# Optimization experiments

Hardware: AMD Instinct MI355X
Metric: run time of the kernel (lower is better)

Reference implementation:

```python
import jax, jax.numpy as jnp
import numpy as np

V = 50257      # num_class
H = 512        # hid_size
EMB = 256      # embedding_size
E = 128        # emb_cond_size
COND_RANGE = (10, 20, 30)
NCSEQ = 100    # num_cond_seq_class
T, B = 64, 32
TC = 32        # cond_seq length


def _gru_scan(x, h0, Wih, Whh, bih, bhh):
    """PyTorch-convention GRU. x: [T,B,in], h0: [B,Hd]. Gate order: r,z,n."""
    Hd = h0.shape[-1]
    xw = jnp.einsum('tbi,gi->tbg', x, Wih) + bih  # [T,B,3H]

    def step(h, xw_t):
        hw = h @ Whh.T + bhh
        r = jax.nn.sigmoid(xw_t[:, :Hd] + hw[:, :Hd])
        z = jax.nn.sigmoid(xw_t[:, Hd:2 * Hd] + hw[:, Hd:2 * Hd])
        n = jnp.tanh(xw_t[:, 2 * Hd:] + r * hw[:, 2 * Hd:])
        hn = (1.0 - z) * n + z * h
        return hn, hn

    hT, outs = jax.lax.scan(step, h0, xw)
    return outs, hT


def setup_inputs() -> dict:
    key = jax.random.key(0)
    ks = jax.random.split(key, 24)
    s = 0.02
    inp = {
        'input_data': jax.random.randint(ks[0], (T, B), 0, V),
        'condition': jnp.stack([jax.random.randint(ks[1 + i], (B,), 0, COND_RANGE[i]) for i in range(3)], 0),
        'cond_seq': jax.random.randint(ks[4], (TC, B), 0, NCSEQ),
        'emb_cond_0': jax.random.normal(ks[5], (COND_RANGE[0], E)) * s,
        'emb_cond_1': jax.random.normal(ks[6], (COND_RANGE[1], E)) * s,
        'emb_cond_2': jax.random.normal(ks[7], (COND_RANGE[2], E)) * s,
        'cond_seq_emb': jax.random.normal(ks[8], (NCSEQ, E)) * s,
        'embedding': jax.random.normal(ks[9], (V, EMB)) * s,
        'attn_W': jax.random.normal(ks[10], (H, E + H)) * s,
        'attn_b': jnp.zeros((H,), jnp.float32),
        'v_W': jax.random.normal(ks[11], (1, H)) * s,
        'gru_Wih': jax.random.normal(ks[12], (3 * H, EMB)) * s,
        'gru_Whh': jax.random.normal(ks[13], (3 * H, H)) * s,
        'gru_bih': jnp.zeros((3 * H,), jnp.float32),
        'gru_bhh': jnp.zeros((3 * H,), jnp.float32),
        'cgru_Wih': jax.random.normal(ks[14], (3 * E, E)) * s,
        'cgru_Whh': jax.random.normal(ks[15], (3 * E, E)) * s,
        'cgru_bih': jnp.zeros((3 * E,), jnp.float32),
        'cgru_bhh': jnp.zeros((3 * E,), jnp.float32),
        'dense_W': jax.random.normal(ks[16], (V, E + EMB + H)) * s,
        'dense_b': jnp.zeros((V,), jnp.float32),
    }
    return inp


def reference(input_data, condition, cond_seq,
              emb_cond_0, emb_cond_1, emb_cond_2, cond_seq_emb, embedding,
              attn_W, attn_b, v_W,
              gru_Wih, gru_Whh, gru_bih, gru_bhh,
              cgru_Wih, cgru_Whh, cgru_bih, cgru_bhh,
              dense_W, dense_b):
    Tl, Bl = input_data.shape
    # conditional embeddings: [num_cond, B, E]
    tables = (emb_cond_0, emb_cond_1, emb_cond_2)
    cond_emb = jnp.stack([tables[i][condition[i]] for i in range(3)], axis=0)
    # conditional sequence GRU encoder: [TC, B, E]
    cseq_in = cond_seq_emb[cond_seq]
    cseq_out, _ = _gru_scan(cseq_in, jnp.zeros((Bl, E), cseq_in.dtype),
                            cgru_Wih, cgru_Whh, cgru_bih, cgru_bhh)
    enc = jnp.concatenate([cond_emb, cseq_out], axis=0)  # [S, B, E]
    enc_b = jnp.transpose(enc, (1, 0, 2))                # [B, S, E]

    # Bahdanau attention: split attn weight into encoder/decoder parts
    W_e = attn_W[:, :E]   # [H, E]
    W_h = attn_W[:, E:]   # [H, H]
    enc_proj = jnp.einsum('bse,he->bsh', enc_b, W_e)     # precompute once

    x_emb = embedding[input_data]                        # [T, B, EMB]
    xw = jnp.einsum('tbi,gi->tbg', x_emb, gru_Wih) + gru_bih  # [T, B, 3H]

    def step(h, inputs):
        xe_t, xw_t = inputs
        # attention against previous hidden h
        score = jnp.tanh(enc_proj + (h @ W_h.T + attn_b)[:, None, :]) @ v_W[0]  # [B,S]
        w = jax.nn.softmax(score, axis=1)
        c = jnp.einsum('bs,bse->be', w, enc_b)           # [B, E]
        # GRU cell
        hw = h @ gru_Whh.T + gru_bhh
        r = jax.nn.sigmoid(xw_t[:, :H] + hw[:, :H])
        z = jax.nn.sigmoid(xw_t[:, H:2 * H] + hw[:, H:2 * H])
        n = jnp.tanh(xw_t[:, 2 * H:] + r * hw[:, 2 * H:])
        hn = (1.0 - z) * n + z * h
        # output head uses context, input embedding and PREVIOUS hidden h
        logits = jnp.concatenate([c, xe_t, h], axis=-1) @ dense_W.T + dense_b
        pred = jax.nn.log_softmax(logits, axis=-1)
        return hn, (pred, w)

    h0 = jnp.zeros((Bl, H), x_emb.dtype)
    hT, (total_pred, weights) = jax.lax.scan(step, h0, (x_emb, xw))
    return total_pred, hT[None, :, :], weights


if __name__ == '__main__':
    out = reference(**setup_inputs())
    print([o.shape for o in out])
```

## Files before the change

### kernel.cpp

```cpp
#include <hip/hip_runtime.h>
#include <hip/hip_bf16.h>
#include <hip/hip_cooperative_groups.h>
#include <math.h>

namespace cg = cooperative_groups;

#define Tt 64
#define Bb 32
#define Hh 512
#define EMBe 256
#define Ee 128
#define Ss 35
#define Vv 50257
#define Kk 896
#define TCc 32
#define VPAD 50304

typedef __bf16 bf16_t;
typedef __bf16 bf16x4 __attribute__((ext_vector_type(4)));
typedef __bf16 bf16x8 __attribute__((ext_vector_type(8)));
typedef float f32x4 __attribute__((ext_vector_type(4)));

__device__ __forceinline__ float sigf(float x){ return 1.f/(1.f + expf(-x)); }

__device__ __forceinline__ void gll16(const void* g, void* l){
  __builtin_amdgcn_global_load_lds(
      (const __attribute__((address_space(1))) unsigned int*)g,
      (__attribute__((address_space(3))) unsigned int*)l, 16, 0, 0);
}

#define DOT4(acc, W_, H_) acc += (W_).x*(H_).x + (W_).y*(H_).y + (W_).z*(H_).z + (W_).w*(H_).w

__global__ void k_cond_emb(const int* __restrict__ cond, const float* __restrict__ t0,
                           const float* __restrict__ t1, const float* __restrict__ t2,
                           float* __restrict__ enc){
  int g = blockIdx.x*blockDim.x + threadIdx.x;
  if (g >= 3*Bb*Ee) return;
  int i = g/(Bb*Ee); int b = (g/Ee)%Bb; int e = g%Ee;
  const float* tbl = (i==0)? t0 : (i==1)? t1 : t2;
  int ci = cond[i*Bb + b];
  enc[(size_t)i*Bb*Ee + b*Ee + e] = tbl[(size_t)ci*Ee + e];
}

__global__ void k_cxw(const int* __restrict__ cond_seq, const float* __restrict__ cemb,
                      const float* __restrict__ Wih, const float* __restrict__ bih,
                      float* __restrict__ cxw){
  __shared__ float es[Ee];
  int row = blockIdx.x; int tid = threadIdx.x;
  int idx = cond_seq[row];
  es[tid] = cemb[(size_t)idx*Ee + tid];
  __syncthreads();
  const float4* hp = (const float4*)es;
  for (int q = 0; q < 3; ++q){
    int g = q*Ee + tid;
    const float4* wr = (const float4*)(Wih + (size_t)g*Ee);
    float acc = bih[g];
    #pragma unroll 8
    for (int k = 0; k < Ee/4; ++k){ float4 w4 = wr[k]; float4 h4 = hp[k]; DOT4(acc, w4, h4); }
    cxw[(size_t)row*(3*Ee) + g] = acc;
  }
}

__global__ void k_xemb(const int* __restrict__ input_data, const float* __restrict__ emb,
                       bf16_t* __restrict__ xe){
  int row = blockIdx.x, tid = threadIdx.x;
  int idx = input_data[row];
  xe[(size_t)row*EMBe + tid] = (bf16_t)emb[(size_t)idx*EMBe + tid];
}

__global__ void k_ctrans(const float* __restrict__ W, float* __restrict__ WT){
  int idx = blockIdx.x*256 + threadIdx.x;
  if (idx >= 3*Ee*Ee) return;
  int g = idx/Ee, k = idx%Ee;
  WT[(size_t)k*(3*Ee) + g] = W[idx];
}

__global__ void k_cseq_scan(const float* __restrict__ cxw, const float* __restrict__ WT,
                            const float* __restrict__ bhh, float* __restrict__ enc){
  __shared__ float hs[Ee];
  int b = blockIdx.x; int j = threadIdx.x;
  hs[j] = 0.f; __syncthreads();
  float b0 = bhh[j], b1 = bhh[Ee+j], b2 = bhh[2*Ee+j];
  for (int t = 0; t < TCc; ++t){
    const float* xp = cxw + ((size_t)t*Bb + b)*(3*Ee);
    float a0=b0, a1=b1, a2=b2;
    #pragma unroll 4
    for (int k = 0; k < Ee; ++k){
      float hk = hs[k];
      const float* wr = WT + (size_t)k*(3*Ee);
      a0 += hk * wr[j];
      a1 += hk * wr[Ee + j];
      a2 += hk * wr[2*Ee + j];
    }
    float r = sigf(xp[j] + a0);
    float z = sigf(xp[Ee + j] + a1);
    float n = tanhf(xp[2*Ee + j] + r*a2);
    float hcur = hs[j];
    float hn = (1.f - z)*n + z*hcur;
    __syncthreads();
    hs[j] = hn;
    enc[(size_t)(3+t)*Bb*Ee + b*Ee + j] = hn;
    __syncthreads();
  }
}

__global__ void k_encproj(const float* __restrict__ enc, const float* __restrict__ attn_W,
                          float* __restrict__ enc_proj){
  __shared__ float es[Ee];
  int blk = blockIdx.x; int tid = threadIdx.x;
  int b = blk/Ss, s = blk%Ss;
  if (tid < Ee) es[tid] = enc[(size_t)s*Bb*Ee + b*Ee + tid];
  __syncthreads();
  const float4* hp = (const float4*)es;
  for (int q = 0; q < 2; ++q){
    int hh = q*256 + tid;
    const float4* wr = (const float4*)(attn_W + (size_t)hh*(Ee+Hh));
    float acc = 0.f;
    #pragma unroll 8
    for (int k = 0; k < Ee/4; ++k){ float4 w4 = wr[k]; float4 h4 = hp[k]; DOT4(acc, w4, h4); }
    enc_proj[(size_t)blk*Hh + hh] = acc;
  }
}

__global__ void k_binit(int* bar){
  int i = threadIdx.x;
  if (i < 256)
    __hip_atomic_store(&bar[i], 0, __ATOMIC_RELAXED, __HIP_MEMORY_SCOPE_AGENT);
}

#define SCAN_BLOCKS 16
#define SCAN_THREADS 384
#define WSL_STRIDE 520
#define HST_STRIDE 520
#define GW_STRIDE 104
#define HSLOT (Bb*Hh)
#define SCAN_LDS (96*WSL_STRIDE*2 + Bb*HST_STRIDE*2 + Bb*GW_STRIDE*4)

__device__ __forceinline__ void poll16(const int* flags, int gen){
  const int* p = flags + ((threadIdx.x & 15))*16;
  for (;;){
    int v = __hip_atomic_load(p, __ATOMIC_RELAXED, __HIP_MEMORY_SCOPE_AGENT);
    if (__all(v >= gen)) break;
    __builtin_amdgcn_s_sleep(1);
  }
}

__global__ __launch_bounds__(SCAN_THREADS) void k_scan_coop(
    const float* __restrict__ xw, const float* __restrict__ Whh,
    const float* __restrict__ bhh, float* __restrict__ h_all,
    bf16_t* __restrict__ hsteps, int* __restrict__ bar){
  extern __shared__ char smem[];
  bf16_t* Wsl = (bf16_t*)smem;
  bf16_t* hst = (bf16_t*)(smem + 96*WSL_STRIDE*2);
  float*  gw  = (float*) (smem + 96*WSL_STRIDE*2 + Bb*HST_STRIDE*2);
  const int tid = threadIdx.x;
  const int blk = blockIdx.x;
  const int c0 = blk*32;
  int* wflag = bar;

  for (int lr = 0; lr < 96; ++lr){
    int g = lr >> 5, i = lr & 31;
    const float* src = Whh + ((size_t)g*Hh + c0 + i)*Hh;
    for (int c = tid; c < Hh; c += SCAN_THREADS)
      Wsl[lr*WSL_STRIDE + c] = (bf16_t)src[c];
  }
  for (int idx = tid; idx < Bb*16; idx += SCAN_THREADS){
    int b = idx >> 4, u = idx & 15;
    __hip_atomic_store((unsigned*)hsteps + ((b*Hh + c0) >> 1) + u, 0u,
                       __ATOMIC_RELAXED, __HIP_MEMORY_SCOPE_AGENT);
    float* hp = &h_all[(size_t)b*Hh + c0 + u*2];
    hp[0] = 0.f; hp[1] = 0.f;
  }

  const int npair = (tid < 128) ? 2 : 1;
  int pb[2], pc[2];
  float bh0[2][2], bh1[2][2], bh2[2][2], hreg[2][2];
  for (int p = 0; p < npair; ++p){
    int pid = tid + p*SCAN_THREADS;
    pb[p] = pid >> 4; pc[p] = (pid & 15)*2;
    for (int c = 0; c < 2; ++c){
      int j = c0 + pc[p] + c;
      bh0[p][c] = bhh[j]; bh1[p][c] = bhh[Hh + j]; bh2[p][c] = bhh[2*Hh + j];
      hreg[p][c] = 0.f;
    }
  }

  __syncthreads();
  if (tid == 0)
    __hip_atomic_store(&wflag[blk*16], 1, __ATOMIC_RELAXED, __HIP_MEMORY_SCOPE_AGENT);

  const int wid = tid >> 6, lane = tid & 63;
  const int l15 = lane & 15, l4 = lane >> 4;

  for (int t = 0; t < Tt; ++t){
    poll16(wflag, t + 1);
    {
      const unsigned long long* hinU = (const unsigned long long*)(hsteps + (size_t)t*HSLOT);
      for (int idx = tid; idx < Bb*Hh/4; idx += SCAN_THREADS){
        unsigned long long v = __hip_atomic_load(hinU + idx, __ATOMIC_RELAXED, __HIP_MEMORY_SCOPE_AGENT);
        int b = idx >> 7, c4 = idx & 127;
        *((unsigned long long*)(hst + (size_t)b*HST_STRIDE) + c4) = v;
      }
    }
    __syncthreads();

    f32x4 acc0 = {0.f,0.f,0.f,0.f}, acc1 = {0.f,0.f,0.f,0.f};
    #pragma unroll
    for (int ks = 0; ks < 16; ++ks){
      bf16x8 bfr = *(const bf16x8*)(Wsl + (wid*16 + l15)*WSL_STRIDE + ks*32 + l4*8);
      bf16x8 a0  = *(const bf16x8*)(hst + l15*HST_STRIDE        + ks*32 + l4*8);
      bf16x8 a1  = *(const bf16x8*)(hst + (16 + l15)*HST_STRIDE + ks*32 + l4*8);
      acc0 = __builtin_amdgcn_mfma_f32_16x16x32_bf16(a0, bfr, acc0, 0, 0, 0);
      acc1 = __builtin_amdgcn_mfma_f32_16x16x32_bf16(a1, bfr, acc1, 0, 0, 0);
    }
    #pragma unroll
    for (int i = 0; i < 4; ++i){
      gw[(l4*4 + i)*GW_STRIDE + wid*16 + l15]        = acc0[i];
      gw[(16 + l4*4 + i)*GW_STRIDE + wid*16 + l15]   = acc1[i];
    }
    __syncthreads();

    unsigned* houtU = (unsigned*)(hsteps + (size_t)(t+1)*HSLOT);
    for (int p = 0; p < npair; ++p){
      int b = pb[p], cl = pc[p];
      const float* xp = xw + ((size_t)t*Bb + b)*(3*Hh);
      float hn2[2];
      #pragma unroll
      for (int c = 0; c < 2; ++c){
        int j = c0 + cl + c;
        float gr = gw[b*GW_STRIDE + cl + c]      + bh0[p][c];
        float gz = gw[b*GW_STRIDE + 32 + cl + c] + bh1[p][c];
        float gn = gw[b*GW_STRIDE + 64 + cl + c] + bh2[p][c];
        float r = sigf(xp[j] + gr);
        float z = sigf(xp[Hh + j] + gz);
        float n = tanhf(xp[2*Hh + j] + r*gn);
        float hn = (1.f - z)*n + z*hreg[p][c];
        hreg[p][c] = hn; hn2[c] = hn;
      }
      unsigned u0 = (unsigned)__builtin_bit_cast(unsigned short, (bf16_t)hn2[0]);
      unsigned u1 = (unsigned)__builtin_bit_cast(unsigned short, (bf16_t)hn2[1]);
      __hip_atomic_store(houtU + ((b*Hh + c0 + cl) >> 1), u0 | (u1 << 16),
                         __ATOMIC_RELAXED, __HIP_MEMORY_SCOPE_AGENT);
    }
    __syncthreads();
    if (tid == 0 && t + 1 < Tt)
      __hip_atomic_store(&wflag[blk*16], t + 2, __ATOMIC_RELAXED, __HIP_MEMORY_SCOPE_AGENT);
    for (int p = 0; p < npair; ++p){
      int b = pb[p], cl = pc[p];
      float* hp = &h_all[((size_t)(t+1)*Bb + b)*Hh + c0 + cl];
      hp[0] = hreg[p][0]; hp[1] = hreg[p][1];
    }
  }
}

#define SG_LDS (256*64*2)
#define SWZ(rowv, uv) (((size_t)(rowv))*64 + ((((uv) ^ ((rowv)&7)))<<3))

template<int KTOT, int LDB>
__global__ __launch_bounds__(256) void k_sgemm(const bf16_t* __restrict__ A,
                                               const float* __restrict__ B,
                                               const float* __restrict__ bias,
                                               float* __restrict__ C, int N){
  extern __shared__ char smem[];
  bf16_t* As = (bf16_t*)smem;
  bf16_t* Ws = As + 128*64;
  const int tid = threadIdx.x, bid = blockIdx.x;
  const int mt = bid & 15, nt = bid >> 4;
  const int m0 = mt*128, n0 = nt*128;
  const int srow = tid >> 1, sub = (tid & 1)*4;
  const int NKK2 = KTOT/64;

  int4 aR[4]; float4 wF[8];
#define SLOADA(KK) { \
    const int4* p = (const int4*)(A + (size_t)(m0 + srow)*KTOT + (KK)*64 + sub*8); \
    aR[0]=p[0]; aR[1]=p[1]; aR[2]=p[2]; aR[3]=p[3]; }
#define SLOADW(KK) { \
    const float4* p = (const float4*)(B + (size_t)(n0 + srow)*LDB + (KK)*64 + sub*8); \
    _Pragma("unroll") for (int r = 0; r < 8; ++r) wF[r] = p[r]; }
#define SSTORES() { \
    _Pragma("unroll") \
    for (int j = 0; j < 4; ++j) \
      *(int4*)(As + SWZ(srow, sub + j)) = aR[j]; \
    _Pragma("unroll") for (int j = 0; j < 4; ++j){ \
      bf16x8 p8; \
      p8[0]=(bf16_t)wF[2*j].x; p8[1]=(bf16_t)wF[2*j].y; p8[2]=(bf16_t)wF[2*j].z; p8[3]=(bf16_t)wF[2*j].w; \
      p8[4]=(bf16_t)wF[2*j+1].x; p8[5]=(bf16_t)wF[2*j+1].y; p8[6]=(bf16_t)wF[2*j+1].z; p8[7]=(bf16_t)wF[2*j+1].w; \
      *(bf16x8*)(Ws + SWZ(srow, sub + j)) = p8; \
    } }

  const int wave = tid >> 6, lane = tid & 63;
  const int l15 = lane & 15, l4 = lane >> 4;
  const int mh = (wave >> 1)*64, nh = (wave & 1)*64;

  f32x4 acc[4][4];
  #pragma unroll
  for (int i = 0; i < 4; ++i)
    #pragma unroll
    for (int j = 0; j < 4; ++j) acc[i][j] = (f32x4){0.f,0.f,0.f,0.f};

  SLOADA(0); SLOADW(0);
  SSTORES();
  __syncthreads();
  for (int kk = 0; kk < NKK2; ++kk){
    if (kk + 1 < NKK2){ SLOADA(kk + 1); SLOADW(kk + 1); }
    #pragma unroll
    for (int k32 = 0; k32 < 2; ++k32){
      const int u = k32*4 + l4;
      bf16x8 aF[4], bF[4];
      #pragma unroll
      for (int mf = 0; mf < 4; ++mf)
        aF[mf] = *(const bf16x8*)(As + SWZ(mh + mf*16 + l15, u));
      #pragma unroll
      for (int nf = 0; nf < 4; ++nf)
        bF[nf] = *(const bf16x8*)(Ws + SWZ(nh + nf*16 + l15, u));
      #pragma unroll
      for (int mf = 0; mf < 4; ++mf)
        #pragma unroll
        for (int nf = 0; nf < 4; ++nf)
          acc[mf][nf] = __builtin_amdgcn_mfma_f32_16x16x32_bf16(aF[mf], bF[nf], acc[mf][nf], 0, 0, 0);
    }
    __syncthreads();
    if (kk + 1 < NKK2){
      SSTORES();
      __syncthreads();
    }
  }
  #pragma unroll
  for (int mf = 0; mf < 4; ++mf){
    #pragma unroll
    for (int nf = 0; nf < 4; ++nf){
      int v = n0 + nh + nf*16 + l15;
      float bv = bias[v];
      int m = m0 + mh + mf*16 + l4*4;
      #pragma unroll
      for (int i = 0; i < 4; ++i)
        C[(size_t)(m + i)*N + v] = acc[mf][nf][i] + bv;
    }
  }
#undef SLOADA
#undef SLOADW
#undef SSTORES
}

__global__ void k_score(const float* __restrict__ hw_attn, const float* __restrict__ enc_proj,
                        const float* __restrict__ enc, const float* __restrict__ vW,
                        float* __restrict__ w_out, float* __restrict__ c_all){
  __shared__ float hws[Hh];
  __shared__ float sc[Ss];
  __shared__ float wsm[Ss];
  int row = blockIdx.x, lane = threadIdx.x;
  int b = row & (Bb-1);
  for (int k = lane; k < Hh; k += 64) hws[k] = hw_attn[(size_t)row*Hh + k];
  __syncthreads();
  for (int s = 0; s < Ss; ++s){
    const float* ep = enc_proj + ((size_t)b*Ss + s)*Hh;
    float acc = 0.f;
    for (int k = lane; k < Hh; k += 64) acc += tanhf(ep[k] + hws[k]) * vW[k];
    #pragma unroll
    for (int off = 32; off > 0; off >>= 1) acc += __shfl_xor(acc, off);
    if (lane == 0) sc[s] = acc;
  }
  __syncthreads();
  float val = (lane < Ss) ? sc[lane] : -3.0e38f;
  float mx = val;
  #pragma unroll
  for (int off = 32; off > 0; off >>= 1) mx = fmaxf(mx, __shfl_xor(mx, off));
  float e = (lane < Ss) ? expf(val - mx) : 0.f;
  float sm = e;
  #pragma unroll
  for (int off = 32; off > 0; off >>= 1) sm += __shfl_xor(sm, off);
  float w = e / sm;
  if (lane < Ss){ w_out[(size_t)row*Ss + lane] = w; wsm[lane] = w; }
  __syncthreads();
  for (int q = 0; q < 2; ++q){
    int ee = q*64 + lane;
    float acc = 0.f;
    #pragma unroll
    for (int s = 0; s < Ss; ++s) acc += wsm[s]*enc[(size_t)s*Bb*Ee + b*Ee + ee];
    c_all[(size_t)row*Ee + ee] = acc;
  }
}

__global__ void k_abuild(const int* __restrict__ input_data, const float* __restrict__ c_all,
                         const float* __restrict__ embedding, const float* __restrict__ h_all,
                         bf16_t* __restrict__ A){
  int row = blockIdx.x, tid = threadIdx.x;
  int xidx = input_data[row];
  bf16_t* Ar = A + (size_t)row*Kk;
  int rs = row & 7;
  for (int col = tid; col < Kk; col += 256){
    float v;
    if (col < Ee) v = c_all[(size_t)row*Ee + col];
    else if (col < Ee + EMBe) v = embedding[(size_t)xidx*EMBe + (col - Ee)];
    else v = h_all[(size_t)row*Hh + (col - Ee - EMBe)];
    int kk = col >> 6, u = (col & 63) >> 3, e = col & 7;
    Ar[(kk << 6) + ((u ^ rs) << 3) + e] = (bf16_t)v;
  }
}

__global__ void k_wconv(const float* __restrict__ Wd, bf16_t* __restrict__ Wb){
  size_t i = ((size_t)blockIdx.x*256 + threadIdx.x)*8;
  if (i >= (size_t)VPAD*Kk) return;
  size_t row = i / Kk;
  int col = (int)(i % Kk);
  bf16x8 o;
  if (row < Vv){
    float4 f0 = *(const float4*)(Wd + i);
    float4 f1 = *(const float4*)(Wd + i + 4);
    o[0]=(bf16_t)f0.x; o[1]=(bf16_t)f0.y; o[2]=(bf16_t)f0.z; o[3]=(bf16_t)f0.w;
    o[4]=(bf16_t)f1.x; o[5]=(bf16_t)f1.y; o[6]=(bf16_t)f1.z; o[7]=(bf16_t)f1.w;
  } else {
    #pragma unroll
    for (int k = 0; k < 8; ++k) o[k] = (bf16_t)0.f;
  }
  int kk = col >> 6, u = (col & 63) >> 3;
  int rs = (int)(row & 7);
  *(bf16x8*)(Wb + row*Kk + (kk << 6) + ((u ^ rs) << 3)) = o;
}

#define BM 128
#define BN 128
#define BK 64
#define NKK (Kk/BK)
#define GEMM_LDS ((BM + BN)*BK*2)

template<int WBF>
__global__ __launch_bounds__(256) void k_gemm7(const bf16_t* __restrict__ A,
                                               const void* __restrict__ Wsrc,
                                               const float* __restrict__ bias,
                                               float* __restrict__ out){
  extern __shared__ char smem[];
  bf16_t* As = (bf16_t*)smem;
  bf16_t* Ws = As + BM*BK;
  const int tid = threadIdx.x;
  const int bid = blockIdx.x;
  const int mt = bid & 15, nt = bid >> 4;
  const int m0 = mt*BM, n0 = nt*BN;
  const int wave = tid >> 6, lane = tid & 63;
  const int l15 = lane & 15, l4 = lane >> 4;
  const int mh = (wave >> 1)*64, nh = (wave & 1)*64;

  f32x4 acc[4][4];
  #pragma unroll
  for (int i = 0; i < 4; ++i)
    #pragma unroll
    for (int j = 0; j < 4; ++j) acc[i][j] = (f32x4){0.f,0.f,0.f,0.f};

  if (WBF){
    const char* Ag = (const char*)A;
    const char* Wg = (const char*)Wsrc;
    char* Asb = (char*)As; char* Wsb = (char*)Ws;
    const int grow = tid >> 3;
    const size_t gcol = (size_t)(tid & 7)*16;
    #pragma unroll
    for (int j = 0; j < 4; ++j){
      gll16(Ag + (size_t)(m0 + j*32 + grow)*(Kk*2) + gcol, Asb + j*4096 + tid*16);
      gll16(Wg + (size_t)(n0 + j*32 + grow)*(Kk*2) + gcol, Wsb + j*4096 + tid*16);
    }
    __syncthreads();
    for (int kk = 0; kk < NKK; ++kk){
      #pragma unroll
      for (int k32 = 0; k32 < 2; ++k32){
        const int u = k32*4 + l4;
        bf16x8 aF[4], bF[4];
        #pragma unroll
        for (int mf = 0; mf < 4; ++mf)
          aF[mf] = *(const bf16x8*)(As + SWZ(mh + mf*16 + l15, u));
        #pragma unroll
        for (int nf = 0; nf < 4; ++nf)
          bF[nf] = *(const bf16x8*)(Ws + SWZ(nh + nf*16 + l15, u));
        #pragma unroll
        for (int mf = 0; mf < 4; ++mf)
          #pragma unroll
          for (int nf = 0; nf < 4; ++nf)
            acc[mf][nf] = __builtin_amdgcn_mfma_f32_16x16x32_bf16(aF[mf], bF[nf], acc[mf][nf], 0, 0, 0);
      }
      __syncthreads();
      if (kk + 1 < NKK){
        size_t ko = (size_t)(kk + 1)*128;
        #pragma unroll
        for (int j = 0; j < 4; ++j){
          gll16(Ag + (size_t)(m0 + j*32 + grow)*(Kk*2) + ko + gcol, Asb + j*4096 + tid*16);
          gll16(Wg + (size_t)(n0 + j*32 + grow)*(Kk*2) + ko + gcol, Wsb + j*4096 + tid*16);
        }
        __syncthreads();
      }
    }
  } else {
    const int srow = tid >> 1, sub = (tid & 1)*4;
    int4 aR[4]; float4 wF[8];
    const float* Wf = (const float*)Wsrc;
#define LOADA(KK) { \
    const int4* p = (const int4*)(A + (size_t)(m0 + srow)*Kk + (KK)*BK + sub*8); \
    aR[0]=p[0]; aR[1]=p[1]; aR[2]=p[2]; aR[3]=p[3]; }
#define LOADW(KK) { \
    int vrow = n0 + srow; \
    if (vrow < Vv){ \
      const float4* p = (const float4*)(Wf + (size_t)vrow*Kk + (KK)*BK + sub*8); \
      _Pragma("unroll") for (int r = 0; r < 8; ++r) wF[r] = p[r]; \
    } else { \
      _Pragma("unroll") for (int r = 0; r < 8; ++r) wF[r] = make_float4(0.f,0.f,0.f,0.f); \
    } }
#define STORES() { \
    _Pragma("unroll") \
    for (int j = 0; j < 4; ++j) \
      *(int4*)(As + (size_t)srow*64 + (size_t)(sub + j)*8) = aR[j]; \
    _Pragma("unroll") for (int j = 0; j < 4; ++j){ \
      bf16x8 p8; \
      p8[0]=(bf16_t)wF[2*j].x; p8[1]=(bf16_t)wF[2*j].y; p8[2]=(bf16_t)wF[2*j].z; p8[3]=(bf16_t)wF[2*j].w; \
      p8[4]=(bf16_t)wF[2*j+1].x; p8[5]=(bf16_t)wF[2*j+1].y; p8[6]=(bf16_t)wF[2*j+1].z; p8[7]=(bf16_t)wF[2*j+1].w; \
      *(bf16x8*)(Ws + SWZ(srow, sub + j)) = p8; \
    } }
    LOADA(0); LOADW(0);
    STORES();
    __syncthreads();
    for (int kk = 0; kk < NKK; ++kk){
      if (kk + 1 < NKK){ LOADA(kk + 1); LOADW(kk + 1); }
      #pragma unroll
      for (int k32 = 0; k32 < 2; ++k32){
        const int u = k32*4 + l4;
        bf16x8 aF[4], bF[4];
        #pragma unroll
        for (int mf = 0; mf < 4; ++mf)
          aF[mf] = *(const bf16x8*)(As + SWZ(mh + mf*16 + l15, u));
        #pragma unroll
        for (int nf = 0; nf < 4; ++nf)
          bF[nf] = *(const bf16x8*)(Ws + SWZ(nh + nf*16 + l15, u));
        #pragma unroll
        for (int mf = 0; mf < 4; ++mf)
          #pragma unroll
          for (int nf = 0; nf < 4; ++nf)
            acc[mf][nf] = __builtin_amdgcn_mfma_f32_16x16x32_bf16(aF[mf], bF[nf], acc[mf][nf], 0, 0, 0);
      }
      __syncthreads();
      if (kk + 1 < NKK){
        STORES();
        __syncthreads();
      }
    }
#undef LOADA
#undef LOADW
#undef STORES
  }
  #pragma unroll
  for (int mf = 0; mf < 4; ++mf){
    #pragma unroll
    for (int nf = 0; nf < 4; ++nf){
      int v = n0 + nh + nf*16 + l15;
      if (v < Vv){
        float bv = bias[v];
        int m = m0 + mh + mf*16 + l4*4;
        #pragma unroll
        for (int i = 0; i < 4; ++i){
          out[(size_t)(m + i)*Vv + v] = acc[mf][nf][i] + bv;
        }
      }
    }
  }
}

__global__ void k_lse(const float* __restrict__ pred, float* __restrict__ lse){
  __shared__ float ms[256], ssum[256];
  int row = blockIdx.x, tid = threadIdx.x;
  const float* p = pred + (size_t)row*Vv;
  int pre = (int)(((16 - (((size_t)p) & 15)) & 15) >> 2);
  float m = -3.0e38f, s = 0.f;
  if (tid < pre){ float x = p[tid]; m = x; s = 1.f; }
  int n4 = (Vv - pre) >> 2;
  const float4* p4 = (const float4*)(p + pre);
  for (int v = tid; v < n4; v += 256){
    float4 x4 = p4[v];
    #pragma unroll
    for (int q = 0; q < 4; ++q){
      float x = (q==0)? x4.x : (q==1)? x4.y : (q==2)? x4.z : x4.w;
      if (x > m){ s = s*expf(m - x) + 1.f; m = x; }
      else s += expf(x - m);
    }
  }
  int tl = pre + n4*4 + tid;
  if (tl < Vv){ float x = p[tl]; if (x > m){ s = s*expf(m - x) + 1.f; m = x; } else s += expf(x - m); }
  ms[tid] = m; ssum[tid] = s;
  __syncthreads();
  for (int off = 128; off > 0; off >>= 1){
    if (tid < off){
      float m2 = ms[tid+off], s2 = ssum[tid+off];
      float m1 = ms[tid],     s1 = ssum[tid];
      if (m2 > m1){ s1 = s1*expf(m1 - m2) + s2; m1 = m2; }
      else s1 += s2*expf(m2 - m1);
      ms[tid] = m1; ssum[tid] = s1;
    }
    __syncthreads();
  }
  if (tid == 0) lse[row] = ms[0] + logf(ssum[0]);
}

__global__ void k_sub(float* __restrict__ pred, const float* __restrict__ lse){
  int row = blockIdx.x, tid = threadIdx.x;
  float l = lse[row];
  float* p = pred + (size_t)row*Vv;
  int pre = (int)(((16 - (((size_t)p) & 15)) & 15) >> 2);
  if (tid < pre) p[tid] -= l;
  int n4 = (Vv - pre) >> 2;
  float4* p4 = (float4*)(p + pre);
  for (int v = tid; v < n4; v += 256){
    float4 x = p4[v];
    x.x -= l; x.y -= l; x.z -= l; x.w -= l;
    p4[v] = x;
  }
  int tl = pre + n4*4 + tid;
  if (tl < Vv) p[tl] -= l;
}

__global__ void k_hT(const float* __restrict__ h_all, float* __restrict__ hT){
  int g = blockIdx.x*256 + threadIdx.x;
  if (g < Bb*Hh) hT[g] = h_all[(size_t)Tt*Bb*Hh + g];
}

extern "C" void kernel_launch(void* const* d_in, const int* in_sizes, int n_in,
                              void* d_out, int out_size, void* d_ws, size_t ws_size,
                              hipStream_t stream){
  const int*   input_data = (const int*)d_in[0];
  const int*   condition  = (const int*)d_in[1];
  const int*   cond_seq   = (const int*)d_in[2];
  const float* emb_c0     = (const float*)d_in[3];
  const float* emb_c1     = (const float*)d_in[4];
  const float* emb_c2     = (const float*)d_in[5];
  const float* cseq_emb   = (const float*)d_in[6];
  const float* embedding  = (const float*)d_in[7];
  const float* attn_W     = (const float*)d_in[8];
  const float* attn_b     = (const float*)d_in[9];
  const float* v_W        = (const float*)d_in[10];
  const float* gru_Wih    = (const float*)d_in[11];
  const float* gru_Whh    = (const float*)d_in[12];
  const float* gru_bih    = (const float*)d_in[13];
  const float* gru_bhh    = (const float*)d_in[14];
  const float* cgru_Wih   = (const float*)d_in[15];
  const float* cgru_Whh   = (const float*)d_in[16];
  const float* cgru_bih   = (const float*)d_in[17];
  const float* cgru_bhh   = (const float*)d_in[18];
  const float* dense_W    = (const float*)d_in[19];
  const float* dense_b    = (const float*)d_in[20];

  float* out    = (float*)d_out;
  float* pred   = out;
  float* hT_out = out + (size_t)Tt*Bb*Vv;
  float* w_out  = hT_out + (size_t)Bb*Hh;

  float* ws       = (float*)d_ws;
  float* h_all    = ws;
  float* xw       = h_all + (size_t)(Tt+1)*Bb*Hh;
  float* cxw      = xw + (size_t)Tt*Bb*3*Hh;
  float* enc      = cxw + (size_t)TCc*Bb*3*Ee;
  float* enc_proj = enc + (size_t)Ss*Bb*Ee;
  float* hw_attn  = enc_proj + (size_t)Bb*Ss*Hh;
  float* c_all    = hw_attn + (size_t)Tt*Bb*Hh;
  float* lse      = c_all + (size_t)Tt*Bb*Ee;
  bf16_t* Abf     = (bf16_t*)(lse + Tt*Bb);
  bf16_t* hsteps  = Abf + (size_t)Tt*Bb*Kk;
  float* WTc      = (float*)(hsteps + (size_t)(Tt+1)*HSLOT);
  int*   bar      = (int*)(WTc + 128*3*Ee);
  bf16_t* xemb    = (bf16_t*)(bar + 256);
  bf16_t* Wb      = xemb + (size_t)Tt*Bb*EMBe;
  size_t need_b   = (size_t)((char*)(Wb + (size_t)VPAD*Kk) - (char*)d_ws);
  bool use_wbf    = (ws_size >= need_b);

  k_cond_emb<<<48, 256, 0, stream>>>(condition, emb_c0, emb_c1, emb_c2, enc);
  k_cxw<<<TCc*Bb, 128, 0, stream>>>(cond_seq, cseq_emb, cgru_Wih, cgru_bih, cxw);
  k_xemb<<<Tt*Bb, 256, 0, stream>>>(input_data, embedding, xemb);
  k_sgemm<EMBe, EMBe><<<16*12, 256, SG_LDS, stream>>>(xemb, gru_Wih, gru_bih, xw, 3*Hh);
  k_ctrans<<<(3*Ee*Ee + 255)/256, 256, 0, stream>>>(cgru_Whh, WTc);
  k_cseq_scan<<<Bb, Ee, 0, stream>>>(cxw, WTc, cgru_bhh, enc);
  k_encproj<<<Bb*Ss, 256, 0, stream>>>(enc, attn_W, enc_proj);
  k_binit<<<1, 256, 0, stream>>>(bar);
  if (use_wbf)
    k_wconv<<<(int)(((size_t)VPAD*Kk/8 + 255)/256), 256, 0, stream>>>(dense_W, Wb);

  (void)hipFuncSetAttribute((const void*)k_scan_coop, hipFuncAttributeMaxDynamicSharedMemorySize, SCAN_LDS);
  {
    void* xw_p = (void*)xw; void* whh_p = (void*)gru_Whh; void* bhh_p = (void*)gru_bhh;
    void* ha_p = (void*)h_all; void* hs_p = (void*)hsteps; void* bar_p = (void*)bar;
    void* args[] = {&xw_p, &whh_p, &bhh_p, &ha_p, &hs_p, &bar_p};
    (void)hipLaunchCooperativeKernel((const void*)k_scan_coop, dim3(SCAN_BLOCKS), dim3(SCAN_THREADS),
                                     args, SCAN_LDS, stream);
  }

  k_sgemm<Hh, (Ee+Hh)><<<16*4, 256, SG_LDS, stream>>>(hsteps, attn_W + Ee, attn_b, hw_attn, Hh);
  k_score<<<Tt*Bb, 64, 0, stream>>>(hw_attn, enc_proj, enc, v_W, w_out, c_all);
  k_abuild<<<Tt*Bb, 256, 0, stream>>>(input_data, c_all, embedding, h_all, Abf);

  (void)hipFuncSetAttribute((const void*)k_gemm7<1>, hipFuncAttributeMaxDynamicSharedMemorySize, GEMM_LDS);
  (void)hipFuncSetAttribute((const void*)k_gemm7<0>, hipFuncAttributeMaxDynamicSharedMemorySize, GEMM_LDS);
  if (use_wbf){
    k_gemm7<1><<<16*((Vv + BN - 1)/BN), 256, GEMM_LDS, stream>>>(Abf, (const void*)Wb, dense_b, pred);
  } else {
    k_gemm7<0><<<16*((Vv + BN - 1)/BN), 256, GEMM_LDS, stream>>>(Abf, (const void*)dense_W, dense_b, pred);
  }

  k_lse<<<Tt*Bb, 256, 0, stream>>>(pred, lse);
  k_sub<<<Tt*Bb, 256, 0, stream>>>(pred, lse);
  k_hT<<<64, 256, 0, stream>>>(h_all, hT_out);
}
```

Measured before the change: 1.777 ms.

## Replace scan flag barrier with NaN-poison polling and overlap dense weight conversion

Drops the per-step flag barrier in the cooperative GRU scan. The hidden-state buffer is now pre-filled with a NaN sentinel, and each block spin-waits on the data itself until the sentinel is overwritten. The dense weight fp32-to-bf16 conversion moves into extra blocks of the same cooperative launch, so it runs concurrently with the 16 latency-bound scan blocks instead of as a separate kernel. The cost is a poison pass over 65 hidden slots, and the scheme relies on a real hidden value never bit-matching the sentinel pattern.

```diff
diff --git a/kernel.cpp b/kernel.cpp
--- a/kernel.cpp
+++ b/kernel.cpp
@@ -20,6 +20,8 @@
 typedef __bf16 bf16x4 __attribute__((ext_vector_type(4)));
 typedef __bf16 bf16x8 __attribute__((ext_vector_type(8)));
 typedef float f32x4 __attribute__((ext_vector_type(4)));
+
+#define POIS32 0x7FC07FC0u
 
 __device__ __forceinline__ float sigf(float x){ return 1.f/(1.f + expf(-x)); }
 
@@ -122,41 +124,64 @@
   }
 }
 
-__global__ void k_binit(int* bar){
-  int i = threadIdx.x;
-  if (i < 256)
-    __hip_atomic_store(&bar[i], 0, __ATOMIC_RELAXED, __HIP_MEMORY_SCOPE_AGENT);
-}
-
-#define SCAN_BLOCKS 16
+#define HSLOT (Bb*Hh)
+
+__global__ void k_poison(bf16_t* __restrict__ hsteps){
+  size_t i = (size_t)blockIdx.x*256 + threadIdx.x;
+  size_t total = (size_t)(Tt+1)*HSLOT/2;
+  if (i >= total) return;
+  unsigned v = (i < HSLOT/2) ? 0u : POIS32;
+  __hip_atomic_store((unsigned*)hsteps + i, v, __ATOMIC_RELAXED, __HIP_MEMORY_SCOPE_AGENT);
+}
+
+#define SCAN_BLOCKS_L 128
+#define SCAN_WORK 16
 #define SCAN_THREADS 384
 #define WSL_STRIDE 520
 #define HST_STRIDE 520
 #define GW_STRIDE 104
-#define HSLOT (Bb*Hh)
 #define SCAN_LDS (96*WSL_STRIDE*2 + Bb*HST_STRIDE*2 + Bb*GW_STRIDE*4)
-
-__device__ __forceinline__ void poll16(const int* flags, int gen){
-  const int* p = flags + ((threadIdx.x & 15))*16;
-  for (;;){
-    int v = __hip_atomic_load(p, __ATOMIC_RELAXED, __HIP_MEMORY_SCOPE_AGENT);
-    if (__all(v >= gen)) break;
-    __builtin_amdgcn_s_sleep(1);
-  }
-}
+#define NCH 11
 
 __global__ __launch_bounds__(SCAN_THREADS) void k_scan_coop(
     const float* __restrict__ xw, const float* __restrict__ Whh,
     const float* __restrict__ bhh, float* __restrict__ h_all,
-    bf16_t* __restrict__ hsteps, int* __restrict__ bar){
+    bf16_t* __restrict__ hsteps, const float* __restrict__ Wd,
+    bf16_t* __restrict__ Wb, int wbf){
   extern __shared__ char smem[];
+  const int tid = threadIdx.x;
+  const int blk = blockIdx.x;
+
+  if (blk >= SCAN_WORK){
+    if (wbf){
+      size_t total = (size_t)VPAD*Kk/8;
+      size_t stride = (size_t)(SCAN_BLOCKS_L - SCAN_WORK)*SCAN_THREADS;
+      for (size_t c = (size_t)(blk - SCAN_WORK)*SCAN_THREADS + tid; c < total; c += stride){
+        size_t i = c*8;
+        size_t row = i / Kk;
+        int col = (int)(i % Kk);
+        bf16x8 o;
+        if (row < Vv){
+          float4 f0 = *(const float4*)(Wd + i);
+          float4 f1 = *(const float4*)(Wd + i + 4);
+          o[0]=(bf16_t)f0.x; o[1]=(bf16_t)f0.y; o[2]=(bf16_t)f0.z; o[3]=(bf16_t)f0.w;
+          o[4]=(bf16_t)f1.x; o[5]=(bf16_t)f1.y; o[6]=(bf16_t)f1.z; o[7]=(bf16_t)f1.w;
+        } else {
+          #pragma unroll
+          for (int k = 0; k < 8; ++k) o[k] = (bf16_t)0.f;
+        }
+        int kk = col >> 6, u = (col & 63) >> 3;
+        int rs = (int)(row & 7);
+        *(bf16x8*)(Wb + row*Kk + (kk << 6) + ((u ^ rs) << 3)) = o;
+      }
+    }
+    return;
+  }
+
   bf16_t* Wsl = (bf16_t*)smem;
   bf16_t* hst = (bf16_t*)(smem + 96*WSL_STRIDE*2);
   float*  gw  = (float*) (smem + 96*WSL_STRIDE*2 + Bb*HST_STRIDE*2);
-  const int tid = threadIdx.x;
-  const int blk = blockIdx.x;
   const int c0 = blk*32;
-  int* wflag = bar;
 
   for (int lr = 0; lr < 96; ++lr){
     int g = lr >> 5, i = lr & 31;
@@ -166,8 +191,6 @@
   }
   for (int idx = tid; idx < Bb*16; idx += SCAN_THREADS){
     int b = idx >> 4, u = idx & 15;
-    __hip_atomic_store((unsigned*)hsteps + ((b*Hh + c0) >> 1) + u, 0u,
-                       __ATOMIC_RELAXED, __HIP_MEMORY_SCOPE_AGENT);
     float* hp = &h_all[(size_t)b*Hh + c0 + u*2];
     hp[0] = 0.f; hp[1] = 0.f;
   }
@@ -184,22 +207,41 @@
       hreg[p][c] = 0.f;
     }
   }
-
   __syncthreads();
-  if (tid == 0)
-    __hip_atomic_store(&wflag[blk*16], 1, __ATOMIC_RELAXED, __HIP_MEMORY_SCOPE_AGENT);
 
   const int wid = tid >> 6, lane = tid & 63;
   const int l15 = lane & 15, l4 = lane >> 4;
 
   for (int t = 0; t < Tt; ++t){
-    poll16(wflag, t + 1);
     {
       const unsigned long long* hinU = (const unsigned long long*)(hsteps + (size_t)t*HSLOT);
-      for (int idx = tid; idx < Bb*Hh/4; idx += SCAN_THREADS){
-        unsigned long long v = __hip_atomic_load(hinU + idx, __ATOMIC_RELAXED, __HIP_MEMORY_SCOPE_AGENT);
-        int b = idx >> 7, c4 = idx & 127;
-        *((unsigned long long*)(hst + (size_t)b*HST_STRIDE) + c4) = v;
+      unsigned long long v[NCH];
+      int nmine = 0;
+      #pragma unroll
+      for (int k = 0; k < NCH; ++k){
+        int idx = tid + k*SCAN_THREADS;
+        if (idx < Bb*Hh/4){
+          v[k] = __hip_atomic_load(hinU + idx, __ATOMIC_RELAXED, __HIP_MEMORY_SCOPE_AGENT);
+          nmine = k + 1;
+        }
+      }
+      #pragma unroll
+      for (int k = 0; k < NCH; ++k){
+        if (k < nmine){
+          int idx = tid + k*SCAN_THREADS;
+          while ((unsigned)v[k] == POIS32 || (unsigned)(v[k] >> 32) == POIS32){
+            __builtin_amdgcn_s_sleep(1);
+            v[k] = __hip_atomic_load(hinU + idx, __ATOMIC_RELAXED, __HIP_MEMORY_SCOPE_AGENT);
+          }
+        }
+      }
+      #pragma unroll
+      for (int k = 0; k < NCH; ++k){
+        if (k < nmine){
+          int idx = tid + k*SCAN_THREADS;
+          int b = idx >> 7, c4 = idx & 127;
+          *((unsigned long long*)(hst + (size_t)b*HST_STRIDE) + c4) = v[k];
+        }
       }
     }
     __syncthreads();
@@ -242,9 +284,6 @@
       __hip_atomic_store(houtU + ((b*Hh + c0 + cl) >> 1), u0 | (u1 << 16),
                          __ATOMIC_RELAXED, __HIP_MEMORY_SCOPE_AGENT);
     }
-    __syncthreads();
-    if (tid == 0 && t + 1 < Tt)
-      __hip_atomic_store(&wflag[blk*16], t + 2, __ATOMIC_RELAXED, __HIP_MEMORY_SCOPE_AGENT);
     for (int p = 0; p < npair; ++p){
       int b = pb[p], cl = pc[p];
       float* hp = &h_all[((size_t)(t+1)*Bb + b)*Hh + c0 + cl];
@@ -396,26 +435,6 @@
     int kk = col >> 6, u = (col & 63) >> 3, e = col & 7;
     Ar[(kk << 6) + ((u ^ rs) << 3) + e] = (bf16_t)v;
   }
-}
-
-__global__ void k_wconv(const float* __restrict__ Wd, bf16_t* __restrict__ Wb){
-  size_t i = ((size_t)blockIdx.x*256 + threadIdx.x)*8;
-  if (i >= (size_t)VPAD*Kk) return;
-  size_t row = i / Kk;
-  int col = (int)(i % Kk);
-  bf16x8 o;
-  if (row < Vv){
-    float4 f0 = *(const float4*)(Wd + i);
-    float4 f1 = *(const float4*)(Wd + i + 4);
-    o[0]=(bf16_t)f0.x; o[1]=(bf16_t)f0.y; o[2]=(bf16_t)f0.z; o[3]=(bf16_t)f0.w;
-    o[4]=(bf16_t)f1.x; o[5]=(bf16_t)f1.y; o[6]=(bf16_t)f1.z; o[7]=(bf16_t)f1.w;
-  } else {
-    #pragma unroll
-    for (int k = 0; k < 8; ++k) o[k] = (bf16_t)0.f;
-  }
-  int kk = col >> 6, u = (col & 63) >> 3;
-  int rs = (int)(row & 7);
-  *(bf16x8*)(Wb + row*Kk + (kk << 6) + ((u ^ rs) << 3)) = o;
 }
 
 #define BM 128
@@ -671,16 +690,19 @@
   k_ctrans<<<(3*Ee*Ee + 255)/256, 256, 0, stream>>>(cgru_Whh, WTc);
   k_cseq_scan<<<Bb, Ee, 0, stream>>>(cxw, WTc, cgru_bhh, enc);
   k_encproj<<<Bb*Ss, 256, 0, stream>>>(enc, attn_W, enc_proj);
-  k_binit<<<1, 256, 0, stream>>>(bar);
-  if (use_wbf)
-    k_wconv<<<(int)(((size_t)VPAD*Kk/8 + 255)/256), 256, 0, stream>>>(dense_W, Wb);
+  {
+    int npb = (int)(((size_t)(Tt+1)*HSLOT/2 + 255)/256);
+    k_poison<<<npb, 256, 0, stream>>>(hsteps);
+  }
 
   (void)hipFuncSetAttribute((const void*)k_scan_coop, hipFuncAttributeMaxDynamicSharedMemorySize, SCAN_LDS);
   {
     void* xw_p = (void*)xw; void* whh_p = (void*)gru_Whh; void* bhh_p = (void*)gru_bhh;
-    void* ha_p = (void*)h_all; void* hs_p = (void*)hsteps; void* bar_p = (void*)bar;
-    void* args[] = {&xw_p, &whh_p, &bhh_p, &ha_p, &hs_p, &bar_p};
-    (void)hipLaunchCooperativeKernel((const void*)k_scan_coop, dim3(SCAN_BLOCKS), dim3(SCAN_THREADS),
+    void* ha_p = (void*)h_all; void* hs_p = (void*)hsteps;
+    void* wd_p = (void*)dense_W; void* wb_p = (void*)Wb;
+    int wbf = use_wbf ? 1 : 0;
+    void* args[] = {&xw_p, &whh_p, &bhh_p, &ha_p, &hs_p, &wd_p, &wb_p, &wbf};
+    (void)hipLaunchCooperativeKernel((const void*)k_scan_coop, dim3(SCAN_BLOCKS_L), dim3(SCAN_THREADS),
                                      args, SCAN_LDS, stream);
   }
 
```

Measured after the change: 1.674 ms. 1.06x faster.
